# Performance work log

Hardware: AMD Instinct MI355X
Metric: run time of the kernel (lower is better)

The kernel has to match this reference:

```python
import jax, jax.numpy as jnp
import numpy as np

EPS = 1e-5
NUM = 16  # number of per-prototype experts


def _layernorm(x, gamma, beta):
    # normalize over last dim; gamma/beta broadcast against x
    mu = jnp.mean(x, axis=-1, keepdims=True)
    var = jnp.var(x, axis=-1, keepdims=True)
    return (x - mu) * jax.lax.rsqrt(var + EPS) * gamma + beta


def setup_inputs() -> dict:
    key = jax.random.key(0)
    ks = jax.random.split(key, 6)
    B, P, D = 2048, 32, 1024
    s = 1.0 / np.sqrt(D)
    return {
        "x": jax.random.normal(ks[0], (B, P, D), dtype=jnp.float32),
        # per-prototype expert params (stacked over expert dim)
        "g_e": jnp.ones((NUM, D), jnp.float32),
        "b_e": jnp.zeros((NUM, D), jnp.float32),
        "W1_e": jax.random.normal(ks[1], (NUM, D, D), jnp.float32) * s,
        "b1_e": jnp.zeros((NUM, D), jnp.float32),
        "W2_e": jax.random.normal(ks[2], (NUM, D, D), jnp.float32) * s,
        "b2_e": jnp.zeros((NUM, D), jnp.float32),
        # shared MLP params for remaining prototypes
        "g_s": jnp.ones((D,), jnp.float32),
        "b_s": jnp.zeros((D,), jnp.float32),
        "W1_s": jax.random.normal(ks[3], (D, D), jnp.float32) * s,
        "b1_s": jnp.zeros((D,), jnp.float32),
        "W2_s": jax.random.normal(ks[4], (D, D), jnp.float32) * s,
        "b2_s": jnp.zeros((D,), jnp.float32),
    }


def reference(x, g_e, b_e, W1_e, b1_e, W2_e, b2_e,
              g_s, b_s, W1_s, b1_s, W2_s, b2_s):
    # x: (B, P, D); first NUM prototypes go through per-prototype experts,
    # the rest through a single shared MLP. Dropout p=0 => identity.
    xe = x[:, :NUM, :]                     # (B, NUM, D)
    y = _layernorm(xe, g_e, b_e)           # per-expert LN params broadcast over B
    h = jnp.einsum('bnd,ndh->bnh', y, W1_e) + b1_e
    h = jax.nn.gelu(h, approximate=False)  # torch nn.GELU default = exact erf
    out_e = jnp.einsum('bnh,nhk->bnk', h, W2_e) + b2_e

    xr = x[:, NUM:, :]                     # (B, P-NUM, D)
    yr = _layernorm(xr, g_s, b_s)
    hr = jax.nn.gelu(yr @ W1_s + b1_s, approximate=False)
    out_s = hr @ W2_s + b2_s

    return jnp.concatenate([out_e, out_s], axis=1)
```

## Files before the change

kernel.cpp:

```cpp
#include <hip/hip_runtime.h>
#include <hip/hip_bf16.h>
#include <cstdint>
#include <math.h>

using u16 = unsigned short;
typedef __attribute__((ext_vector_type(8))) short bf16x8;
typedef __attribute__((ext_vector_type(4))) float f32x4;

#define BM 128
#define BN 128
#define BK 32

static __device__ __forceinline__ u16 f2bf(float f) {
    union { float f; unsigned int u; } v; v.f = f;
    return (u16)((v.u + 0x7FFFu + ((v.u >> 16) & 1u)) >> 16);
}

typedef const __attribute__((address_space(1))) unsigned int* gptr_t;
typedef __attribute__((address_space(3))) unsigned int* lptr_t;

static __device__ __forceinline__ void load_lds16(const void* g, void* l) {
    __builtin_amdgcn_global_load_lds((gptr_t)g, (lptr_t)l, 16, 0, 0);
}

__global__ __launch_bounds__(256)
void wconv(const float* __restrict__ W1e, const float* __restrict__ W1s,
           const float* __restrict__ W2e, const float* __restrict__ W2s,
           u16* __restrict__ Wt)
{
    const int mat = blockIdx.z;
    const float* src;
    if (mat < 17) src = (mat < 16) ? (W1e + (size_t)mat * 1048576) : W1s;
    else {
        const int m2 = mat - 17;
        src = (m2 < 16) ? (W2e + (size_t)m2 * 1048576) : W2s;
    }
    u16* dst = Wt + (size_t)mat * 1048576;

    __shared__ float tile[32][33];
    const int tx = threadIdx.x & 31, ty = threadIdx.x >> 5;
    const int c0 = blockIdx.x * 32, r0 = blockIdx.y * 32;

#pragma unroll
    for (int j = 0; j < 32; j += 8)
        tile[ty + j][tx] = src[(size_t)(r0 + ty + j) * 1024 + c0 + tx];
    __syncthreads();
#pragma unroll
    for (int j = 0; j < 32; j += 8)
        dst[(size_t)(c0 + ty + j) * 1024 + r0 + tx] = f2bf(tile[tx][ty + j]);
}

__global__ __launch_bounds__(256)
void ln_kernel(const float* __restrict__ x,
               const float* __restrict__ g_e, const float* __restrict__ b_e,
               const float* __restrict__ g_s, const float* __restrict__ b_s,
               u16* __restrict__ Yg)
{
    const int row  = blockIdx.x * 4 + (threadIdx.x >> 6);
    const int lane = threadIdx.x & 63;
    const int b = row >> 5, p = row & 31;

    const float4* x4 = (const float4*)(x + (size_t)row * 1024) + lane * 4;
    float4 v[4];
    float sum = 0.f, ssq = 0.f;
#pragma unroll
    for (int i = 0; i < 4; i++) {
        v[i] = x4[i];
        sum += v[i].x + v[i].y + v[i].z + v[i].w;
        ssq += v[i].x * v[i].x + v[i].y * v[i].y + v[i].z * v[i].z + v[i].w * v[i].w;
    }
#pragma unroll
    for (int off = 32; off > 0; off >>= 1) {
        sum += __shfl_xor(sum, off);
        ssq += __shfl_xor(ssq, off);
    }
    const float mean = sum * (1.0f / 1024.0f);
    const float var  = ssq * (1.0f / 1024.0f) - mean * mean;
    const float rstd = rsqrtf(var + 1e-5f);

    const float4* g4 = (const float4*)((p < 16) ? (g_e + p * 1024) : g_s) + lane * 4;
    const float4* b4 = (const float4*)((p < 16) ? (b_e + p * 1024) : b_s) + lane * 4;

    __attribute__((aligned(16))) u16 o[16];
#pragma unroll
    for (int i = 0; i < 4; i++) {
        const float4 g = g4[i], bb = b4[i];
        o[i * 4 + 0] = f2bf((v[i].x - mean) * rstd * g.x + bb.x);
        o[i * 4 + 1] = f2bf((v[i].y - mean) * rstd * g.y + bb.y);
        o[i * 4 + 2] = f2bf((v[i].z - mean) * rstd * g.z + bb.z);
        o[i * 4 + 3] = f2bf((v[i].w - mean) * rstd * g.w + bb.w);
    }
    u16* dst = Yg + ((size_t)p * 2048 + b) * 1024 + lane * 16;
    ((uint4*)dst)[0] = ((const uint4*)o)[0];
    ((uint4*)dst)[1] = ((const uint4*)o)[1];
}

template <int STAGE>
__global__ __launch_bounds__(256, 2)
void gemm_ffn(const u16* __restrict__ Abase, const u16* __restrict__ Wt,
              const float* __restrict__ bias_e, const float* __restrict__ bias_s,
              u16* __restrict__ Hout, float* __restrict__ Fout)
{
    const int p = blockIdx.z;
    const u16* Ap = Abase + (size_t)p * (2048u * 1024u);
    const u16* Bp = Wt + (size_t)((p < 16) ? p : 16) * (1024u * 1024u);
    const float* bias = (p < 16) ? (bias_e + p * 1024) : bias_s;

    const int m0 = blockIdx.y * BM;
    const int n0 = blockIdx.x * BN;

    __shared__ u16 Als[BM * BK];
    __shared__ u16 Bls[BN * BK];

    const int t = threadIdx.x;
    const int w = t >> 6, l = t & 63;
    const int wm = (w >> 1) * 64, wn = (w & 1) * 64;
    const int lr = l & 15, kq = l >> 4;
    const int srow = t >> 2;
    const int sch  = (t & 3) * 8;

    f32x4 acc[4][4];
#pragma unroll
    for (int i = 0; i < 4; i++)
#pragma unroll
        for (int j = 0; j < 4; j++)
            acc[i][j] = (f32x4){0.f, 0.f, 0.f, 0.f};

    for (int k0 = 0; k0 < 1024; k0 += BK) {
#pragma unroll
        for (int r = 0; r < 2; r++) {
            const u16* ga = Ap + (size_t)(m0 + r * 64 + srow) * 1024 + (k0 + sch);
            const u16* gb = Bp + (size_t)(n0 + r * 64 + srow) * 1024 + (k0 + sch);
            load_lds16(ga, Als + (r * 256 + t) * 8);
            load_lds16(gb, Bls + (r * 256 + t) * 8);
        }
        __syncthreads();

        bf16x8 af[4], bfv[4];
#pragma unroll
        for (int i = 0; i < 4; i++)
            af[i] = *(const bf16x8*)(Als + (wm + i * 16 + lr) * BK + kq * 8);
#pragma unroll
        for (int j = 0; j < 4; j++)
            bfv[j] = *(const bf16x8*)(Bls + (wn + j * 16 + lr) * BK + kq * 8);
#pragma unroll
        for (int i = 0; i < 4; i++)
#pragma unroll
            for (int j = 0; j < 4; j++)
                acc[i][j] = __builtin_amdgcn_mfma_f32_16x16x32_bf16(af[i], bfv[j], acc[i][j], 0, 0, 0);
        __syncthreads();
    }

    float bv[4];
#pragma unroll
    for (int j = 0; j < 4; j++) bv[j] = bias[n0 + wn + j * 16 + lr];

#pragma unroll
    for (int i = 0; i < 4; i++) {
#pragma unroll
        for (int r = 0; r < 4; r++) {
            const int row = m0 + wm + i * 16 + kq * 4 + r;
#pragma unroll
            for (int j = 0; j < 4; j++) {
                const int col = n0 + wn + j * 16 + lr;
                float v2 = acc[i][j][r] + bv[j];
                if (STAGE == 1) {
                    v2 = 0.5f * v2 * (1.0f + erff(v2 * 0.70710678118654752f));
                    Hout[(size_t)p * (2048u * 1024u) + (size_t)row * 1024 + col] = f2bf(v2);
                } else {
                    Fout[((size_t)row * 32 + p) * 1024 + col] = v2;
                }
            }
        }
    }
}

extern "C" void kernel_launch(void* const* d_in, const int* in_sizes, int n_in,
                              void* d_out, int out_size, void* d_ws, size_t ws_size,
                              hipStream_t stream)
{
    const float* x    = (const float*)d_in[0];
    const float* g_e  = (const float*)d_in[1];
    const float* b_e  = (const float*)d_in[2];
    const float* W1_e = (const float*)d_in[3];
    const float* b1_e = (const float*)d_in[4];
    const float* W2_e = (const float*)d_in[5];
    const float* b2_e = (const float*)d_in[6];
    const float* g_s  = (const float*)d_in[7];
    const float* b_s  = (const float*)d_in[8];
    const float* W1_s = (const float*)d_in[9];
    const float* b1_s = (const float*)d_in[10];
    const float* W2_s = (const float*)d_in[11];
    const float* b2_s = (const float*)d_in[12];
    float* out = (float*)d_out;

    u16* Wt = (u16*)d_ws;
    u16* Yg = Wt + (size_t)34 * 1024 * 1024;
    u16* Hg = Yg + (size_t)32 * 2048 * 1024;

    wconv<<<dim3(32, 32, 34), 256, 0, stream>>>(W1_e, W1_s, W2_e, W2_s, Wt);
    ln_kernel<<<16384, 256, 0, stream>>>(x, g_e, b_e, g_s, b_s, Yg);
    gemm_ffn<1><<<dim3(8, 16, 32), 256, 0, stream>>>(Yg, Wt, b1_e, b1_s, Hg, nullptr);
    gemm_ffn<2><<<dim3(8, 16, 32), 256, 0, stream>>>(Hg, Wt + (size_t)17 * 1024 * 1024,
                                                     b2_e, b2_s, nullptr, out);
}
```

Measured before the change: 1.004 ms.

## Rewrite FFN GEMM as 256x256 tile, 8-wave, double-buffered swizzled LDS pipeline

Replaces the 128x128x32 single-buffer GEMM with a 256x256 tile per 512-thread block, BK=64, using double-buffered LDS with XOR-swizzled layout and staged global->LDS loads interleaved with MFMA phases. It adds explicit barrier pinning, vmcnt waits, s_setprio around MFMA clusters, and a block-id remap for XCD locality. The aim is to hide memory latency, cut LDS bank conflicts and raise arithmetic intensity. In exchange it uses far more registers and LDS and depends on hand-placed waits being correct.

```diff
diff --git a/kernel.cpp b/kernel.cpp
--- a/kernel.cpp
+++ b/kernel.cpp
@@ -7,10 +7,6 @@
 typedef __attribute__((ext_vector_type(8))) short bf16x8;
 typedef __attribute__((ext_vector_type(4))) float f32x4;
 
-#define BM 128
-#define BN 128
-#define BK 32
-
 static __device__ __forceinline__ u16 f2bf(float f) {
     union { float f; unsigned int u; } v; v.f = f;
     return (u16)((v.u + 0x7FFFu + ((v.u >> 16) & 1u)) >> 16);
@@ -21,6 +17,12 @@
 
 static __device__ __forceinline__ void load_lds16(const void* g, void* l) {
     __builtin_amdgcn_global_load_lds((gptr_t)g, (lptr_t)l, 16, 0, 0);
+}
+
+static __device__ __forceinline__ void barrier_pin() {
+    __builtin_amdgcn_sched_barrier(0);
+    asm volatile("s_barrier" ::: "memory");
+    __builtin_amdgcn_sched_barrier(0);
 }
 
 __global__ __launch_bounds__(256)
@@ -95,75 +97,167 @@
     ((uint4*)dst)[1] = ((const uint4*)o)[1];
 }
 
+static __device__ __forceinline__ void stage_half(const u16* gb, u16* lb, int tid) {
+#pragma unroll
+    for (int j = 0; j < 2; j++) {
+        const int g = tid + j * 512;
+        const int r = g >> 3;
+        const int c = (g & 7) ^ (r & 7);
+        load_lds16(gb + (size_t)r * 1024 + c * 8, lb + (size_t)g * 8);
+    }
+}
+
+static __device__ __forceinline__ bf16x8 ld_frag(const u16* h, int row, int slot) {
+    return *(const bf16x8*)(h + row * 64 + slot * 8);
+}
+
+#define MFMA_BF16 __builtin_amdgcn_mfma_f32_16x16x32_bf16
+
 template <int STAGE>
-__global__ __launch_bounds__(256, 2)
+__global__ __launch_bounds__(512, 2)
 void gemm_ffn(const u16* __restrict__ Abase, const u16* __restrict__ Wt,
               const float* __restrict__ bias_e, const float* __restrict__ bias_s,
               u16* __restrict__ Hout, float* __restrict__ Fout)
 {
-    const int p = blockIdx.z;
+    const int d   = blockIdx.x;
+    const int vid = (d & 7) * 128 + (d >> 3);
+    const int p   = vid >> 5;
+    const int rem = vid & 31;
+    const int m0  = (rem >> 2) * 256;
+    const int n0  = (rem & 3) * 256;
+
     const u16* Ap = Abase + (size_t)p * (2048u * 1024u);
     const u16* Bp = Wt + (size_t)((p < 16) ? p : 16) * (1024u * 1024u);
     const float* bias = (p < 16) ? (bias_e + p * 1024) : bias_s;
 
-    const int m0 = blockIdx.y * BM;
-    const int n0 = blockIdx.x * BN;
-
-    __shared__ u16 Als[BM * BK];
-    __shared__ u16 Bls[BN * BK];
-
-    const int t = threadIdx.x;
-    const int w = t >> 6, l = t & 63;
-    const int wm = (w >> 1) * 64, wn = (w & 1) * 64;
+    __shared__ u16 lds[2][2][2][8192];
+
+    const int tid = threadIdx.x;
+    const int w = tid >> 6, l = tid & 63;
     const int lr = l & 15, kq = l >> 4;
-    const int srow = t >> 2;
-    const int sch  = (t & 3) * 8;
-
-    f32x4 acc[4][4];
-#pragma unroll
-    for (int i = 0; i < 4; i++)
+    const int wmh = w >> 2;
+    const int wq  = w & 3;
+    const int wnh = wq >> 1;
+    const int bnb = (wq & 1) * 64;
+    const int sl0 = kq ^ (lr & 7);
+    const int sl1 = sl0 ^ 4;
+
+    f32x4 acc[8][4];
+#pragma unroll
+    for (int i = 0; i < 8; i++)
 #pragma unroll
         for (int j = 0; j < 4; j++)
             acc[i][j] = (f32x4){0.f, 0.f, 0.f, 0.f};
 
-    for (int k0 = 0; k0 < 1024; k0 += BK) {
-#pragma unroll
-        for (int r = 0; r < 2; r++) {
-            const u16* ga = Ap + (size_t)(m0 + r * 64 + srow) * 1024 + (k0 + sch);
-            const u16* gb = Bp + (size_t)(n0 + r * 64 + srow) * 1024 + (k0 + sch);
-            load_lds16(ga, Als + (r * 256 + t) * 8);
-            load_lds16(gb, Bls + (r * 256 + t) * 8);
-        }
-        __syncthreads();
-
-        bf16x8 af[4], bfv[4];
-#pragma unroll
-        for (int i = 0; i < 4; i++)
-            af[i] = *(const bf16x8*)(Als + (wm + i * 16 + lr) * BK + kq * 8);
-#pragma unroll
-        for (int j = 0; j < 4; j++)
-            bfv[j] = *(const bf16x8*)(Bls + (wn + j * 16 + lr) * BK + kq * 8);
-#pragma unroll
-        for (int i = 0; i < 4; i++)
-#pragma unroll
-            for (int j = 0; j < 4; j++)
-                acc[i][j] = __builtin_amdgcn_mfma_f32_16x16x32_bf16(af[i], bfv[j], acc[i][j], 0, 0, 0);
-        __syncthreads();
+    stage_half(Ap + (size_t)(m0      ) * 1024,      &lds[0][0][0][0], tid);
+    stage_half(Ap + (size_t)(m0 + 128) * 1024,      &lds[0][0][1][0], tid);
+    stage_half(Bp + (size_t)(n0      ) * 1024,      &lds[0][1][0][0], tid);
+    stage_half(Bp + (size_t)(n0 + 128) * 1024,      &lds[0][1][1][0], tid);
+    stage_half(Bp + (size_t)(n0      ) * 1024 + 64, &lds[1][1][0][0], tid);
+    stage_half(Bp + (size_t)(n0 + 128) * 1024 + 64, &lds[1][1][1][0], tid);
+    asm volatile("s_waitcnt vmcnt(4)" ::: "memory");
+    barrier_pin();
+
+    bf16x8 a[4][2], b[4][2];
+
+    for (int t = 0; t < 16; ++t) {
+        const int sl = t & 1, ot = sl ^ 1;
+        const u16* hA = &lds[sl][0][wmh][0];
+        const u16* hB = &lds[sl][1][wnh][0];
+
+#pragma unroll
+        for (int i = 0; i < 4; ++i) {
+            a[i][0] = ld_frag(hA, i * 16 + lr, sl0);
+            a[i][1] = ld_frag(hA, i * 16 + lr, sl1);
+        }
+#pragma unroll
+        for (int j = 0; j < 2; ++j) {
+            b[j][0] = ld_frag(hB, bnb + j * 16 + lr, sl0);
+            b[j][1] = ld_frag(hB, bnb + j * 16 + lr, sl1);
+        }
+        if (t < 15)
+            stage_half(Ap + (size_t)m0 * 1024 + (t + 1) * 64, &lds[ot][0][0][0], tid);
+        barrier_pin();
+        __builtin_amdgcn_s_setprio(1);
+#pragma unroll
+        for (int i = 0; i < 4; ++i)
+#pragma unroll
+            for (int j = 0; j < 2; ++j) {
+                acc[i][j] = MFMA_BF16(a[i][0], b[j][0], acc[i][j], 0, 0, 0);
+                acc[i][j] = MFMA_BF16(a[i][1], b[j][1], acc[i][j], 0, 0, 0);
+            }
+        __builtin_amdgcn_s_setprio(0);
+        barrier_pin();
+
+#pragma unroll
+        for (int j = 0; j < 2; ++j) {
+            b[2 + j][0] = ld_frag(hB, bnb + (2 + j) * 16 + lr, sl0);
+            b[2 + j][1] = ld_frag(hB, bnb + (2 + j) * 16 + lr, sl1);
+        }
+        if (t < 15)
+            stage_half(Ap + (size_t)(m0 + 128) * 1024 + (t + 1) * 64, &lds[ot][0][1][0], tid);
+        barrier_pin();
+        __builtin_amdgcn_s_setprio(1);
+#pragma unroll
+        for (int i = 0; i < 4; ++i)
+#pragma unroll
+            for (int j = 0; j < 2; ++j) {
+                acc[i][2 + j] = MFMA_BF16(a[i][0], b[2 + j][0], acc[i][2 + j], 0, 0, 0);
+                acc[i][2 + j] = MFMA_BF16(a[i][1], b[2 + j][1], acc[i][2 + j], 0, 0, 0);
+            }
+        __builtin_amdgcn_s_setprio(0);
+        barrier_pin();
+
+#pragma unroll
+        for (int i = 0; i < 4; ++i) {
+            a[i][0] = ld_frag(hA, (4 + i) * 16 + lr, sl0);
+            a[i][1] = ld_frag(hA, (4 + i) * 16 + lr, sl1);
+        }
+        if (t < 14)
+            stage_half(Bp + (size_t)n0 * 1024 + (t + 2) * 64, &lds[sl][1][0][0], tid);
+        barrier_pin();
+        __builtin_amdgcn_s_setprio(1);
+#pragma unroll
+        for (int i = 0; i < 4; ++i)
+#pragma unroll
+            for (int j = 0; j < 2; ++j) {
+                acc[4 + i][j] = MFMA_BF16(a[i][0], b[j][0], acc[4 + i][j], 0, 0, 0);
+                acc[4 + i][j] = MFMA_BF16(a[i][1], b[j][1], acc[4 + i][j], 0, 0, 0);
+            }
+        __builtin_amdgcn_s_setprio(0);
+        barrier_pin();
+
+        if (t < 14)
+            stage_half(Bp + (size_t)(n0 + 128) * 1024 + (t + 2) * 64, &lds[sl][1][1][0], tid);
+        barrier_pin();
+        __builtin_amdgcn_s_setprio(1);
+#pragma unroll
+        for (int i = 0; i < 4; ++i)
+#pragma unroll
+            for (int j = 0; j < 2; ++j) {
+                acc[4 + i][2 + j] = MFMA_BF16(a[i][0], b[2 + j][0], acc[4 + i][2 + j], 0, 0, 0);
+                acc[4 + i][2 + j] = MFMA_BF16(a[i][1], b[2 + j][1], acc[4 + i][2 + j], 0, 0, 0);
+            }
+        __builtin_amdgcn_s_setprio(0);
+        if (t < 14) asm volatile("s_waitcnt vmcnt(4)" ::: "memory");
+        else        asm volatile("s_waitcnt vmcnt(0)" ::: "memory");
+        barrier_pin();
     }
 
     float bv[4];
 #pragma unroll
-    for (int j = 0; j < 4; j++) bv[j] = bias[n0 + wn + j * 16 + lr];
-
-#pragma unroll
-    for (int i = 0; i < 4; i++) {
-#pragma unroll
-        for (int r = 0; r < 4; r++) {
-            const int row = m0 + wm + i * 16 + kq * 4 + r;
-#pragma unroll
-            for (int j = 0; j < 4; j++) {
-                const int col = n0 + wn + j * 16 + lr;
-                float v2 = acc[i][j][r] + bv[j];
+    for (int j = 0; j < 4; ++j) bv[j] = bias[n0 + wq * 64 + j * 16 + lr];
+
+#pragma unroll
+    for (int mi = 0; mi < 8; ++mi) {
+        const int rbase = m0 + wmh * 128 + mi * 16 + kq * 4;
+#pragma unroll
+        for (int r = 0; r < 4; ++r) {
+            const int row = rbase + r;
+#pragma unroll
+            for (int nj = 0; nj < 4; ++nj) {
+                const int col = n0 + wq * 64 + nj * 16 + lr;
+                float v2 = acc[mi][nj][r] + bv[nj];
                 if (STAGE == 1) {
                     v2 = 0.5f * v2 * (1.0f + erff(v2 * 0.70710678118654752f));
                     Hout[(size_t)p * (2048u * 1024u) + (size_t)row * 1024 + col] = f2bf(v2);
@@ -200,7 +294,7 @@
 
     wconv<<<dim3(32, 32, 34), 256, 0, stream>>>(W1_e, W1_s, W2_e, W2_s, Wt);
     ln_kernel<<<16384, 256, 0, stream>>>(x, g_e, b_e, g_s, b_s, Yg);
-    gemm_ffn<1><<<dim3(8, 16, 32), 256, 0, stream>>>(Yg, Wt, b1_e, b1_s, Hg, nullptr);
-    gemm_ffn<2><<<dim3(8, 16, 32), 256, 0, stream>>>(Hg, Wt + (size_t)17 * 1024 * 1024,
-                                                     b2_e, b2_s, nullptr, out);
-}
+    gemm_ffn<1><<<dim3(1024), 512, 0, stream>>>(Yg, Wt, b1_e, b1_s, Hg, nullptr);
+    gemm_ffn<2><<<dim3(1024), 512, 0, stream>>>(Hg, Wt + (size_t)17 * 1024 * 1024,
+                                                b2_e, b2_s, nullptr, out);
+}
```

Result: faster. 924.0 us (-8.0%).
